# Kernel optimization log

Measured on AMD Instinct MI355X. Metric: run time of the kernel, lower is better.

Reference implementation:

```python
import math
import jax, jax.numpy as jnp
import numpy as np

D_MODEL = 128
NUM_HEADS = 8
FACTOR = 5


def setup_inputs() -> dict:
    key = jax.random.key(0)
    ks = jax.random.split(key, 9)
    B, L, dm = 2, 4096, D_MODEL
    s = 1.0 / math.sqrt(dm)
    return {
        "x": jax.random.normal(ks[0], (B, L, dm), dtype=jnp.float32),
        "Wq": jax.random.normal(ks[1], (dm, dm), dtype=jnp.float32) * s,
        "bq": jnp.zeros((dm,), jnp.float32),
        "Wk": jax.random.normal(ks[2], (dm, dm), dtype=jnp.float32) * s,
        "bk": jnp.zeros((dm,), jnp.float32),
        "Wv": jax.random.normal(ks[3], (dm, dm), dtype=jnp.float32) * s,
        "bv": jnp.zeros((dm,), jnp.float32),
        "Wo": jax.random.normal(ks[4], (dm, dm), dtype=jnp.float32) * s,
        "bo": jnp.zeros((dm,), jnp.float32),
    }


def reference(x, Wq, bq, Wk, bk, Wv, bv, Wo, bo):
    B, L, dm = x.shape
    H = NUM_HEADS
    D = dm // H
    inv_sqrt_d = 1.0 / math.sqrt(D)

    def split_heads(t):  # [B,L,dm] -> [B,H,L,D]
        return t.reshape(B, L, H, D).transpose(0, 2, 1, 3)

    Q = split_heads(x @ Wq + bq)
    K = split_heads(x @ Wk + bk)
    V = split_heads(x @ Wv + bv)

    # sample_k = min(L_K, int(log(L_K) * factor)); L is static under jit
    sample_k = min(L, int(math.log(L) * FACTOR))

    # _prob_QK: full scores, per-query stable exp, mean over queries, top-k keys
    scores_full = jnp.einsum("bhqd,bhkd->bhqk", Q, K) * inv_sqrt_d  # [B,H,L,L]
    m = jnp.max(scores_full, axis=-1, keepdims=True)
    e = jnp.exp(scores_full - m)
    mean_attn = jnp.mean(e, axis=2)  # [B,H,L_K]
    _, idx = jax.lax.top_k(mean_attn, sample_k)  # [B,H,sample_k]

    # gather sampled keys/values along the key axis
    Ks = jnp.take_along_axis(K, idx[..., None], axis=2)  # [B,H,s,D]
    Vs = jnp.take_along_axis(V, idx[..., None], axis=2)

    attn = jax.nn.softmax(jnp.einsum("bhqd,bhsd->bhqs", Q, Ks) * inv_sqrt_d, axis=-1)
    out = jnp.einsum("bhqs,bhsd->bhqd", attn, Vs)  # [B,H,L,D]
    out = out.transpose(0, 2, 1, 3).reshape(B, L, dm)
    return out @ Wo + bo
```

## Files before the change

### kernel.cpp

```cpp
#include <hip/hip_runtime.h>
#include <hip/hip_bf16.h>

#define L 4096
#define DM 128
#define NH 8
#define HD 16
#define NBH 16
#define SK 41
#define NSPLIT 8
#define SLICE (L/NSPLIT)
#define KK (SLICE/16)
#define QSCALE 0.36067376022224085f

typedef __attribute__((ext_vector_type(8))) short s16x8;
typedef __attribute__((ext_vector_type(4))) float f32x4;

#define MFMA16(A,B,C) __builtin_amdgcn_mfma_f32_16x16x32_bf16(A,B,C,0,0,0)

__device__ __forceinline__ float bf2f(unsigned short h){ return __uint_as_float(((unsigned)h)<<16); }
__device__ __forceinline__ unsigned short f2bf(float f){
  unsigned u = __float_as_uint(f);
  u += 0x7FFFu + ((u>>16)&1u);
  return (unsigned short)(u>>16);
}
__device__ __forceinline__ float fast_exp2(float x){
  float r;
  asm("v_exp_f32 %0, %1" : "=v"(r) : "v"(x));
  return r;
}

__global__ __launch_bounds__(256) void prep(
    const float* __restrict__ x,
    const float* __restrict__ Wq, const float* __restrict__ Wk,
    const float* __restrict__ Wv, const float* __restrict__ Wo,
    unsigned short* __restrict__ Xh, unsigned short* __restrict__ Xl,
    unsigned short* __restrict__ Wph, unsigned short* __restrict__ Wpl)
{
  const int t = threadIdx.x;
  const int blk = blockIdx.x;
  if (blk < 1024){
    const long base = (long)blk*1024 + t*4;
    float4 v = *(const float4*)(x + base);
    unsigned short h[4], lo[4];
    h[0]=f2bf(v.x); lo[0]=f2bf(v.x - bf2f(h[0]));
    h[1]=f2bf(v.y); lo[1]=f2bf(v.y - bf2f(h[1]));
    h[2]=f2bf(v.z); lo[2]=f2bf(v.z - bf2f(h[2]));
    h[3]=f2bf(v.w); lo[3]=f2bf(v.w - bf2f(h[3]));
    *(uint2*)(Xh+base) = *(uint2*)h;
    *(uint2*)(Xl+base) = *(uint2*)lo;
  } else {
    const int e = (blk-1024)*256 + t;
    const int p = e >> 14;
    const int idx = e & 16383;
    const int j = idx & 7;
    const int f = idx >> 3;
    const int n = f & 127;
    const int kcg = f >> 7;
    const int k = (kcg>>1)*16 + (kcg&1)*8 + j;
    const float* W = (p==0)?Wq:((p==1)?Wk:((p==2)?Wv:Wo));
    const float v = W[k*128 + n];
    const unsigned short h = f2bf(v);
    Wph[e] = h;
    Wpl[e] = f2bf(v - bf2f(h));
  }
}

__global__ __launch_bounds__(256) void proj_mfma(
    const unsigned short* __restrict__ Xh, const unsigned short* __restrict__ Xl,
    const unsigned short* __restrict__ Wph, const unsigned short* __restrict__ Wpl,
    const float* __restrict__ bq, const float* __restrict__ bk, const float* __restrict__ bv,
    unsigned short* __restrict__ Qh, unsigned short* __restrict__ Ql,
    unsigned short* __restrict__ Kh, unsigned short* __restrict__ Kl,
    float* __restrict__ Vo)
{
  const int p = blockIdx.y;
  const float* __restrict__ bias = (p==0)?bq:((p==1)?bk:bv);
  __shared__ __align__(16) unsigned short wh[16384];
  __shared__ __align__(16) unsigned short wl[16384];
  const int t = threadIdx.x;
  {
    const uint4* gh = (const uint4*)(Wph + (long)p*16384);
    const uint4* gl = (const uint4*)(Wpl + (long)p*16384);
    uint4* sh = (uint4*)wh; uint4* sl = (uint4*)wl;
#pragma unroll
    for (int i=0;i<8;++i){ sh[t + i*256] = gh[t + i*256]; sl[t + i*256] = gl[t + i*256]; }
  }
  __syncthreads();
  const int w = t>>6, l = t&63;
  const int lc = l&15, g = l>>4;
  const int mbase = blockIdx.x*64 + w*16;
  f32x4 acc[8];
#pragma unroll
  for (int nt=0;nt<8;++nt){ acc[nt][0]=0.f; acc[nt][1]=0.f; acc[nt][2]=0.f; acc[nt][3]=0.f; }
  const unsigned short* __restrict__ Asrc = (g<2)? Xh : Xl;
  const int koff = (g&1)*8;
  for (int kc=0; kc<8; ++kc){
    s16x8 a = *(const s16x8*)(Asrc + ((long)(mbase + lc))*128 + kc*16 + koff);
#pragma unroll
    for (int nt=0;nt<8;++nt){
      const int fi = (kc*2+(g&1))*128 + nt*16 + lc;
      s16x8 b1 = ((const s16x8*)wh)[fi];
      s16x8 b2 = ((const s16x8*)wl)[fi];
      acc[nt] = MFMA16(a, b1, acc[nt]);
      acc[nt] = MFMA16(a, b2, acc[nt]);
    }
  }
#pragma unroll
  for (int nt=0;nt<8;++nt){
    const float bb = bias[nt*16 + lc];
#pragma unroll
    for (int r=0;r<4;++r){
      const int row = mbase + g*4 + r;
      float v = acc[nt][r] + bb;
      const int b = row>>12, li = row&4095;
      const long o = (((long)(b*NH + nt))*L + li)*HD + lc;
      if (p==2){
        Vo[o] = v;
      } else {
        if (p==0) v *= QSCALE;
        const unsigned short h = f2bf(v);
        const unsigned short lo2 = f2bf(v - bf2f(h));
        if (p==0){ Qh[o]=h; Ql[o]=lo2; } else { Kh[o]=h; Kl[o]=lo2; }
      }
    }
  }
}

__global__ __launch_bounds__(256) void rowmax_k(
    const unsigned short* __restrict__ Qh, const unsigned short* __restrict__ Ql,
    const unsigned short* __restrict__ Kh, const unsigned short* __restrict__ Kl,
    float* __restrict__ mpart)
{
  const int bh = blockIdx.y, qt = blockIdx.x, ks = blockIdx.z;
  const int t = threadIdx.x, w = t>>6, l = t&63;
  const int half = (l>>4)&1, part = l>>5, lc = l&15;
  __shared__ __align__(16) unsigned short khs[SLICE*HD];
  __shared__ __align__(16) unsigned short kls[SLICE*HD];
  {
    const uint4* gh = (const uint4*)(Kh + ((long)bh*L + ks*SLICE)*HD);
    const uint4* gl = (const uint4*)(Kl + ((long)bh*L + ks*SLICE)*HD);
    uint4* sh = (uint4*)khs; uint4* sl = (uint4*)kls;
#pragma unroll
    for (int i=0;i<4;++i){ sh[t + i*256] = gh[t + i*256]; sl[t + i*256] = gl[t + i*256]; }
  }
  s16x8 aq[4];
  {
    const unsigned short* Qsrc = part ? Ql : Qh;
#pragma unroll
    for (int m=0;m<4;++m){
      const int row = qt*256 + w*64 + m*16 + lc;
      aq[m] = *(const s16x8*)(Qsrc + (((long)bh*L + row)*HD) + half*8);
    }
  }
  __syncthreads();
  f32x4 fz; fz[0]=0.f; fz[1]=0.f; fz[2]=0.f; fz[3]=0.f;
  f32x4 rmax[4];
#pragma unroll
  for (int m=0;m<4;++m){ rmax[m][0]=rmax[m][1]=rmax[m][2]=rmax[m][3]=-3.4e38f; }
  const int boff = lc*HD + half*8;
  f32x4 accA[4], accB[4];
  {
    s16x8 b1 = *(const s16x8*)(khs + boff);
    s16x8 b2 = *(const s16x8*)(kls + boff);
#pragma unroll
    for (int m=0;m<4;++m){ accA[m] = MFMA16(aq[m], b2, fz); accA[m] = MFMA16(aq[m], b1, accA[m]); }
  }
  for (int kk=0; kk<KK-2; kk+=2){
    {
      s16x8 b1 = *(const s16x8*)(khs + (kk+1)*256 + boff);
      s16x8 b2 = *(const s16x8*)(kls + (kk+1)*256 + boff);
#pragma unroll
      for (int m=0;m<4;++m){ accB[m] = MFMA16(aq[m], b2, fz); accB[m] = MFMA16(aq[m], b1, accB[m]); }
    }
#pragma unroll
    for (int m=0;m<4;++m)
#pragma unroll
      for (int r=0;r<4;++r) rmax[m][r] = fmaxf(rmax[m][r], accA[m][r]);
    {
      s16x8 b1 = *(const s16x8*)(khs + (kk+2)*256 + boff);
      s16x8 b2 = *(const s16x8*)(kls + (kk+2)*256 + boff);
#pragma unroll
      for (int m=0;m<4;++m){ accA[m] = MFMA16(aq[m], b2, fz); accA[m] = MFMA16(aq[m], b1, accA[m]); }
    }
#pragma unroll
    for (int m=0;m<4;++m)
#pragma unroll
      for (int r=0;r<4;++r) rmax[m][r] = fmaxf(rmax[m][r], accB[m][r]);
  }
  {
    s16x8 b1 = *(const s16x8*)(khs + (KK-1)*256 + boff);
    s16x8 b2 = *(const s16x8*)(kls + (KK-1)*256 + boff);
#pragma unroll
    for (int m=0;m<4;++m){ accB[m] = MFMA16(aq[m], b2, fz); accB[m] = MFMA16(aq[m], b1, accB[m]); }
  }
#pragma unroll
  for (int m=0;m<4;++m)
#pragma unroll
    for (int r=0;r<4;++r) rmax[m][r] = fmaxf(fmaxf(rmax[m][r], accA[m][r]), accB[m][r]);
#pragma unroll
  for (int m=0;m<4;++m){
#pragma unroll
    for (int r=0;r<4;++r){
      float v = rmax[m][r];
      v = fmaxf(v, __shfl_xor(v, 1));
      v = fmaxf(v, __shfl_xor(v, 2));
      v = fmaxf(v, __shfl_xor(v, 4));
      v = fmaxf(v, __shfl_xor(v, 8));
      rmax[m][r] = v;
    }
  }
  if (lc == 0){
    const int q4 = l>>4;
#pragma unroll
    for (int m=0;m<4;++m){
#pragma unroll
      for (int r=0;r<4;++r){
        const int row = qt*256 + w*64 + m*16 + q4*4 + r;
        mpart[((long)ks*NBH + bh)*L + row] = rmax[m][r];
      }
    }
  }
}

__global__ __launch_bounds__(256) void colexp_k(
    const unsigned short* __restrict__ Kh, const unsigned short* __restrict__ Kl,
    const unsigned short* __restrict__ Qh, const unsigned short* __restrict__ Ql,
    const float* __restrict__ mpart, float* __restrict__ cspart)
{
  const int bh = blockIdx.y, kt = blockIdx.x, qs = blockIdx.z;
  const int t = threadIdx.x, w = t>>6, l = t&63;
  const int half = (l>>4)&1, part = l>>5, lc = l&15;
  __shared__ __align__(16) unsigned short qhs[SLICE*HD];
  __shared__ __align__(16) unsigned short qls[SLICE*HD];
  __shared__ float ws_s[SLICE];
  {
    const uint4* gh = (const uint4*)(Qh + ((long)bh*L + qs*SLICE)*HD);
    const uint4* gl = (const uint4*)(Ql + ((long)bh*L + qs*SLICE)*HD);
    uint4* sh = (uint4*)qhs; uint4* sl = (uint4*)qls;
#pragma unroll
    for (int i=0;i<4;++i){ sh[t + i*256] = gh[t + i*256]; sl[t + i*256] = gl[t + i*256]; }
#pragma unroll
    for (int rr=0; rr<2; ++rr){
      const int tq = t + rr*256;
      const long qi = (long)bh*L + qs*SLICE + tq;
      float m = -3.4e38f;
#pragma unroll
      for (int p=0;p<NSPLIT;++p) m = fmaxf(m, mpart[(long)p*NBH*L + qi]);
      ws_s[tq] = fast_exp2(-m);
    }
  }
  s16x8 ak[4];
  {
    const unsigned short* Ksrc = part ? Kl : Kh;
#pragma unroll
    for (int m=0;m<4;++m){
      const int key = kt*256 + w*64 + m*16 + lc;
      ak[m] = *(const s16x8*)(Ksrc + (((long)bh*L + key)*HD) + half*8);
    }
  }
  __syncthreads();
  f32x4 fz; fz[0]=0.f; fz[1]=0.f; fz[2]=0.f; fz[3]=0.f;
  f32x4 csum[4];
#pragma unroll
  for (int m=0;m<4;++m){ csum[m][0]=0.f; csum[m][1]=0.f; csum[m][2]=0.f; csum[m][3]=0.f; }
  const int boff = lc*HD + half*8;
  f32x4 accA[4], accB[4];
  {
    s16x8 b1 = *(const s16x8*)(qhs + boff);
    s16x8 b2 = *(const s16x8*)(qls + boff);
#pragma unroll
    for (int m=0;m<4;++m){ accA[m] = MFMA16(ak[m], b2, fz); accA[m] = MFMA16(ak[m], b1, accA[m]); }
  }
  for (int kk=0; kk<KK-2; kk+=2){
    {
      s16x8 b1 = *(const s16x8*)(qhs + (kk+1)*256 + boff);
      s16x8 b2 = *(const s16x8*)(qls + (kk+1)*256 + boff);
#pragma unroll
      for (int m=0;m<4;++m){ accB[m] = MFMA16(ak[m], b2, fz); accB[m] = MFMA16(ak[m], b1, accB[m]); }
    }
    {
      const float cw = ws_s[kk*16 + lc];
#pragma unroll
      for (int m=0;m<4;++m)
#pragma unroll
        for (int r=0;r<4;++r)
          csum[m][r] = fmaf(fast_exp2(accA[m][r]), cw, csum[m][r]);
    }
    {
      s16x8 b1 = *(const s16x8*)(qhs + (kk+2)*256 + boff);
      s16x8 b2 = *(const s16x8*)(qls + (kk+2)*256 + boff);
#pragma unroll
      for (int m=0;m<4;++m){ accA[m] = MFMA16(ak[m], b2, fz); accA[m] = MFMA16(ak[m], b1, accA[m]); }
    }
    {
      const float cw = ws_s[(kk+1)*16 + lc];
#pragma unroll
      for (int m=0;m<4;++m)
#pragma unroll
        for (int r=0;r<4;++r)
          csum[m][r] = fmaf(fast_exp2(accB[m][r]), cw, csum[m][r]);
    }
  }
  {
    s16x8 b1 = *(const s16x8*)(qhs + (KK-1)*256 + boff);
    s16x8 b2 = *(const s16x8*)(qls + (KK-1)*256 + boff);
#pragma unroll
    for (int m=0;m<4;++m){ accB[m] = MFMA16(ak[m], b2, fz); accB[m] = MFMA16(ak[m], b1, accB[m]); }
  }
  {
    const float cwA = ws_s[(KK-2)*16 + lc];
    const float cwB = ws_s[(KK-1)*16 + lc];
#pragma unroll
    for (int m=0;m<4;++m)
#pragma unroll
      for (int r=0;r<4;++r){
        csum[m][r] = fmaf(fast_exp2(accA[m][r]), cwA, csum[m][r]);
        csum[m][r] = fmaf(fast_exp2(accB[m][r]), cwB, csum[m][r]);
      }
  }
#pragma unroll
  for (int m=0;m<4;++m){
#pragma unroll
    for (int r=0;r<4;++r){
      float v = csum[m][r];
      v += __shfl_xor(v, 1);
      v += __shfl_xor(v, 2);
      v += __shfl_xor(v, 4);
      v += __shfl_xor(v, 8);
      csum[m][r] = v;
    }
  }
  if (lc == 0){
    const int k4 = l>>4;
#pragma unroll
    for (int m=0;m<4;++m){
#pragma unroll
      for (int r=0;r<4;++r){
        const int key = kt*256 + w*64 + m*16 + k4*4 + r;
        cspart[((long)qs*NBH + bh)*L + key] = csum[m][r];
      }
    }
  }
}

__global__ __launch_bounds__(256) void topk_gather(
    const float* __restrict__ cspart,
    const unsigned short* __restrict__ Kh, const unsigned short* __restrict__ Kl,
    const float* __restrict__ V,
    float* __restrict__ Ks, float* __restrict__ Vs)
{
  const int bh = blockIdx.x;
  const int t = threadIdx.x;
  __shared__ float vals[4096];
  __shared__ unsigned hist[2048];
  __shared__ unsigned suf[256];
  __shared__ int meta[4];
  __shared__ int sel[SK];
  __shared__ int sorted[SK];
  __shared__ int tiei[4096];

  for (int i=t; i<1024; i+=256){
    float4 s = {0.f,0.f,0.f,0.f};
#pragma unroll
    for (int p=0;p<NSPLIT;++p){
      float4 v = *(const float4*)(cspart + ((long)p*NBH + bh)*L + i*4);
      s.x += v.x; s.y += v.y; s.z += v.z; s.w += v.w;
    }
    *(float4*)&vals[i*4] = s;
  }
  __syncthreads();

  int target = SK;
  unsigned B1 = 0, P2 = 0, T = 0;
#pragma unroll
  for (int pass=0; pass<3; ++pass){
    const int nb = (pass<2) ? 2048 : 1024;
    const int chunk = nb >> 8;
    for (int i=t;i<nb;i+=256) hist[i]=0u;
    __syncthreads();
    for (int i=t;i<4096;i+=256){
      const unsigned u = __float_as_uint(vals[i]);
      bool ok; int bk;
      if (pass==0){ ok = true;              bk = (int)(u>>21); }
      else if (pass==1){ ok = ((u>>21)==B1); bk = (int)((u>>10)&0x7FFu); }
      else { ok = ((u>>10)==P2);            bk = (int)(u&0x3FFu); }
      if (ok) atomicAdd(&hist[bk], 1u);
    }
    __syncthreads();
    {
      unsigned c=0;
#pragma unroll
      for (int b=0;b<8;++b) if (b<chunk) c += hist[t*chunk+b];
      suf[t]=c;
    }
    __syncthreads();
    for (int off=1; off<256; off<<=1){
      unsigned add = (t+off<256)? suf[t+off] : 0u;
      __syncthreads();
      suf[t] += add;
      __syncthreads();
    }
    {
      const unsigned mysuf = suf[t];
      const unsigned nxt = (t==255)?0u:suf[t+1];
      if (mysuf >= (unsigned)target && nxt < (unsigned)target){
        unsigned running = nxt;
        for (int b=t*chunk+chunk-1; b>=t*chunk; --b){
          const unsigned h = hist[b];
          if (running + h >= (unsigned)target){ meta[0]=b; meta[1]=(int)running; break; }
          running += h;
        }
      }
    }
    __syncthreads();
    const unsigned B = (unsigned)meta[0];
    target -= meta[1];
    if (pass==0) B1 = B;
    else if (pass==1) P2 = (B1<<11)|B;
    else T = (P2<<10)|B;
    __syncthreads();
  }
  if (t==0){ meta[2]=0; meta[3]=0; }
  __syncthreads();
  for (int i=t;i<4096;i+=256){
    const unsigned u = __float_as_uint(vals[i]);
    if (u > T){ int p = atomicAdd(&meta[2],1); sel[p]=i; }
    else if (u == T){ int p = atomicAdd(&meta[3],1); tiei[p]=i; }
  }
  __syncthreads();
  const int ngt = meta[2];
  const int ntie = meta[3];
  for (int j=t; j<ntie; j+=256){
    const int x = tiei[j];
    int rk=0;
    for (int k=0;k<ntie;++k) rk += (tiei[k] < x);
    if (rk < target) sel[ngt+rk] = x;
  }
  __syncthreads();
  if (t<SK){
    int x=sel[t]; int rk=0;
    for (int j=0;j<SK;++j) rk += (sel[j]<x);
    sorted[rk]=x;
  }
  __syncthreads();
  for (int i=t;i<SK*HD;i+=256){
    const int j=i>>4, dd=i&15;
    const int key=sorted[j];
    const long src=((long)bh*L+key)*HD+dd;
    Ks[(long)bh*SK*HD+i]=bf2f(Kh[src])+bf2f(Kl[src]);
    Vs[(long)bh*SK*HD+i]=V[src];
  }
}

__global__ __launch_bounds__(256) void sattn(
    const unsigned short* __restrict__ Qh, const unsigned short* __restrict__ Ql,
    const float* __restrict__ Ks, const float* __restrict__ Vs,
    unsigned short* __restrict__ AOh, unsigned short* __restrict__ AOl)
{
  const int bh = blockIdx.y, qb = blockIdx.x;
  const int t = threadIdx.x;
  __shared__ float ks[SK*HD], vs[SK*HD];
  for (int i=t; i<SK*HD; i+=256){
    ks[i] = Ks[(long)bh*SK*HD + i];
    vs[i] = Vs[(long)bh*SK*HD + i];
  }
  __syncthreads();
  const int q = qb*128 + (t>>1);
  const int half = t&1;
  const long qo = ((long)bh*L + q)*HD;
  float qv[16];
  {
    s16x8 h0 = *(const s16x8*)(Qh+qo);
    s16x8 h1 = *(const s16x8*)(Qh+qo+8);
    s16x8 l0 = *(const s16x8*)(Ql+qo);
    s16x8 l1 = *(const s16x8*)(Ql+qo+8);
#pragma unroll
    for (int d=0; d<8; ++d){
      qv[d]   = bf2f((unsigned short)h0[d]) + bf2f((unsigned short)l0[d]);
      qv[d+8] = bf2f((unsigned short)h1[d]) + bf2f((unsigned short)l1[d]);
    }
  }
  float sc[21];
#pragma unroll
  for (int i=0;i<21;++i){
    const int j = half + 2*i;
    if (j < SK){
      float4 k0 = *(const float4*)&ks[j*HD+0];
      float4 k1 = *(const float4*)&ks[j*HD+4];
      float4 k2 = *(const float4*)&ks[j*HD+8];
      float4 k3 = *(const float4*)&ks[j*HD+12];
      float s = qv[0]*k0.x;
      s = fmaf(qv[1],k0.y,s); s = fmaf(qv[2],k0.z,s); s = fmaf(qv[3],k0.w,s);
      s = fmaf(qv[4],k1.x,s); s = fmaf(qv[5],k1.y,s); s = fmaf(qv[6],k1.z,s); s = fmaf(qv[7],k1.w,s);
      s = fmaf(qv[8],k2.x,s); s = fmaf(qv[9],k2.y,s); s = fmaf(qv[10],k2.z,s); s = fmaf(qv[11],k2.w,s);
      s = fmaf(qv[12],k3.x,s); s = fmaf(qv[13],k3.y,s); s = fmaf(qv[14],k3.z,s); s = fmaf(qv[15],k3.w,s);
      sc[i] = s;
    } else {
      sc[i] = -3.4e38f;
    }
  }
  float m = sc[0];
#pragma unroll
  for (int i=1;i<21;++i) m = fmaxf(m, sc[i]);
  float lrun = 0.f, out[16];
#pragma unroll
  for (int d=0; d<16; ++d) out[d] = 0.f;
#pragma unroll
  for (int i=0;i<21;++i){
    const int j = half + 2*i;
    const float p = fast_exp2(sc[i] - m);
    lrun += p;
    if (j < SK){
      float4 v0 = *(const float4*)&vs[j*HD+0];
      float4 v1 = *(const float4*)&vs[j*HD+4];
      float4 v2 = *(const float4*)&vs[j*HD+8];
      float4 v3 = *(const float4*)&vs[j*HD+12];
      out[0]=fmaf(p,v0.x,out[0]); out[1]=fmaf(p,v0.y,out[1]); out[2]=fmaf(p,v0.z,out[2]); out[3]=fmaf(p,v0.w,out[3]);
      out[4]=fmaf(p,v1.x,out[4]); out[5]=fmaf(p,v1.y,out[5]); out[6]=fmaf(p,v1.z,out[6]); out[7]=fmaf(p,v1.w,out[7]);
      out[8]=fmaf(p,v2.x,out[8]); out[9]=fmaf(p,v2.y,out[9]); out[10]=fmaf(p,v2.z,out[10]); out[11]=fmaf(p,v2.w,out[11]);
      out[12]=fmaf(p,v3.x,out[12]); out[13]=fmaf(p,v3.y,out[13]); out[14]=fmaf(p,v3.z,out[14]); out[15]=fmaf(p,v3.w,out[15]);
    }
  }
  const float mo = __shfl_xor(m, 1);
  const float lo = __shfl_xor(lrun, 1);
  const float mm = fmaxf(m, mo);
  const float cs_ = fast_exp2(m - mm);
  const float co_ = fast_exp2(mo - mm);
  const float ltot = fmaf(lrun, cs_, lo*co_);
  const float inv = 1.f / ltot;
#pragma unroll
  for (int d=0; d<16; ++d){
    const float ov = __shfl_xor(out[d], 1);
    out[d] = fmaf(out[d]*cs_, inv, ov*co_*inv);
  }
  if (half == 0){
    const int b = bh>>3, h = bh&7;
    const long row = (long)b*L + q;
    unsigned short hv[16], lv[16];
#pragma unroll
    for (int d=0; d<16; ++d){
      const float v = out[d];
      hv[d] = f2bf(v);
      lv[d] = f2bf(v - bf2f(hv[d]));
    }
    unsigned short* oh = AOh + row*DM + h*HD;
    unsigned short* ol = AOl + row*DM + h*HD;
    *(uint4*)(oh)   = *(uint4*)(hv);
    *(uint4*)(oh+8) = *(uint4*)(hv+8);
    *(uint4*)(ol)   = *(uint4*)(lv);
    *(uint4*)(ol+8) = *(uint4*)(lv+8);
  }
}

__global__ __launch_bounds__(256) void outproj_mfma(
    const unsigned short* __restrict__ AOh, const unsigned short* __restrict__ AOl,
    const unsigned short* __restrict__ Wph, const unsigned short* __restrict__ Wpl,
    const float* __restrict__ bo, float* __restrict__ out)
{
  __shared__ __align__(16) unsigned short wh[16384];
  __shared__ __align__(16) unsigned short wl[16384];
  const int t = threadIdx.x;
  {
    const uint4* gh = (const uint4*)(Wph + (long)3*16384);
    const uint4* gl = (const uint4*)(Wpl + (long)3*16384);
    uint4* sh = (uint4*)wh; uint4* sl = (uint4*)wl;
#pragma unroll
    for (int i=0;i<8;++i){ sh[t + i*256] = gh[t + i*256]; sl[t + i*256] = gl[t + i*256]; }
  }
  __syncthreads();
  const int w = t>>6, l = t&63;
  const int lc = l&15, g = l>>4;
  const int mbase = blockIdx.x*64 + w*16;
  f32x4 acc[8];
#pragma unroll
  for (int nt=0;nt<8;++nt){ acc[nt][0]=0.f; acc[nt][1]=0.f; acc[nt][2]=0.f; acc[nt][3]=0.f; }
  const unsigned short* __restrict__ Asrc = (g<2)? AOh : AOl;
  const int koff = (g&1)*8;
  for (int kc=0; kc<8; ++kc){
    s16x8 a = *(const s16x8*)(Asrc + ((long)(mbase + lc))*128 + kc*16 + koff);
#pragma unroll
    for (int nt=0;nt<8;++nt){
      const int fi = (kc*2+(g&1))*128 + nt*16 + lc;
      s16x8 b1 = ((const s16x8*)wh)[fi];
      s16x8 b2 = ((const s16x8*)wl)[fi];
      acc[nt] = MFMA16(a, b1, acc[nt]);
      acc[nt] = MFMA16(a, b2, acc[nt]);
    }
  }
#pragma unroll
  for (int nt=0;nt<8;++nt){
    const float bb = bo[nt*16 + lc];
#pragma unroll
    for (int r=0;r<4;++r){
      const int row = mbase + g*4 + r;
      out[(long)row*DM + nt*16 + lc] = acc[nt][r] + bb;
    }
  }
}

extern "C" void kernel_launch(void* const* d_in, const int* in_sizes, int n_in,
                              void* d_out, int out_size, void* d_ws, size_t ws_size,
                              hipStream_t stream)
{
  const float* x  = (const float*)d_in[0];
  const float* Wq = (const float*)d_in[1];
  const float* bq = (const float*)d_in[2];
  const float* Wk = (const float*)d_in[3];
  const float* bk = (const float*)d_in[4];
  const float* Wv = (const float*)d_in[5];
  const float* bv = (const float*)d_in[6];
  const float* Wo = (const float*)d_in[7];
  const float* bo = (const float*)d_in[8];
  float* out = (float*)d_out;

  char* wsp = (char*)d_ws;
  size_t o = 0;
  auto alloc = [&](size_t bytes)->char*{
    char* p = wsp + o; o += (bytes + 255) & ~(size_t)255; return p;
  };
  unsigned short* Qh = (unsigned short*)alloc((size_t)NBH*L*HD*2);
  unsigned short* Ql = (unsigned short*)alloc((size_t)NBH*L*HD*2);
  unsigned short* Kh = (unsigned short*)alloc((size_t)NBH*L*HD*2);
  unsigned short* Kl = (unsigned short*)alloc((size_t)NBH*L*HD*2);
  float* Vv    = (float*)alloc((size_t)NBH*L*HD*4);
  float* mpart = (float*)alloc((size_t)NSPLIT*NBH*L*4);
  float* cspart= (float*)alloc((size_t)NSPLIT*NBH*L*4);
  float* Ks    = (float*)alloc((size_t)NBH*SK*HD*4);
  float* Vs    = (float*)alloc((size_t)NBH*SK*HD*4);
  unsigned short* Xh  = (unsigned short*)alloc((size_t)2*L*DM*2);
  unsigned short* Xl  = (unsigned short*)alloc((size_t)2*L*DM*2);
  unsigned short* AOh = (unsigned short*)alloc((size_t)2*L*DM*2);
  unsigned short* AOl = (unsigned short*)alloc((size_t)2*L*DM*2);
  unsigned short* Wph = (unsigned short*)alloc((size_t)4*16384*2);
  unsigned short* Wpl = (unsigned short*)alloc((size_t)4*16384*2);

  prep<<<1280,256,0,stream>>>(x,Wq,Wk,Wv,Wo,Xh,Xl,Wph,Wpl);
  proj_mfma<<<dim3(128,3),256,0,stream>>>(Xh,Xl,Wph,Wpl,bq,bk,bv,Qh,Ql,Kh,Kl,Vv);
  rowmax_k<<<dim3(16,16,NSPLIT),256,0,stream>>>(Qh,Ql,Kh,Kl,mpart);
  colexp_k<<<dim3(16,16,NSPLIT),256,0,stream>>>(Kh,Kl,Qh,Ql,mpart,cspart);
  topk_gather<<<16,256,0,stream>>>(cspart,Kh,Kl,Vv,Ks,Vs);
  sattn<<<dim3(32,16),256,0,stream>>>(Qh,Ql,Ks,Vs,AOh,AOl);
  outproj_mfma<<<128,256,0,stream>>>(AOh,AOl,Wph,Wpl,bo,out);
}
```

Baseline: 132.1 us.

## Use bit-trick exp2 for column sums, then re-rank top candidates exactly

Replaces the hardware exp in the full column-exp pass with a cheap integer bit-trick exp2 approximation. Top-k then selects 192 candidate keys from these approximate sums. A new kernel recomputes exact column sums for only those candidates, and a final kernel picks the true top 41. The aim is to cut transcendental cost in the dominant L×L pass while keeping selection exact. The cost is two extra kernel launches, and a true top-41 key could fall outside the approximate top 192.

```diff
diff --git a/kernel.cpp b/kernel.cpp
--- a/kernel.cpp
+++ b/kernel.cpp
@@ -7,6 +7,7 @@
 #define HD 16
 #define NBH 16
 #define SK 41
+#define NC 192
 #define NSPLIT 8
 #define SLICE (L/NSPLIT)
 #define KK (SLICE/16)
@@ -27,6 +28,11 @@
   float r;
   asm("v_exp_f32 %0, %1" : "=v"(r) : "v"(x));
   return r;
+}
+__device__ __forceinline__ float approx_exp2(float x){
+  x = fmaxf(x, -120.f);
+  const float y = fmaf(x, 8388608.f, 1064986823.f);
+  return __int_as_float((int)y);
 }
 
 __global__ __launch_bounds__(256) void prep(
@@ -284,7 +290,7 @@
       for (int m=0;m<4;++m)
 #pragma unroll
         for (int r=0;r<4;++r)
-          csum[m][r] = fmaf(fast_exp2(accA[m][r]), cw, csum[m][r]);
+          csum[m][r] = fmaf(approx_exp2(accA[m][r]), cw, csum[m][r]);
     }
     {
       s16x8 b1 = *(const s16x8*)(qhs + (kk+2)*256 + boff);
@@ -298,7 +304,7 @@
       for (int m=0;m<4;++m)
 #pragma unroll
         for (int r=0;r<4;++r)
-          csum[m][r] = fmaf(fast_exp2(accB[m][r]), cw, csum[m][r]);
+          csum[m][r] = fmaf(approx_exp2(accB[m][r]), cw, csum[m][r]);
     }
   }
   {
@@ -314,8 +320,8 @@
     for (int m=0;m<4;++m)
 #pragma unroll
       for (int r=0;r<4;++r){
-        csum[m][r] = fmaf(fast_exp2(accA[m][r]), cwA, csum[m][r]);
-        csum[m][r] = fmaf(fast_exp2(accB[m][r]), cwB, csum[m][r]);
+        csum[m][r] = fmaf(approx_exp2(accA[m][r]), cwA, csum[m][r]);
+        csum[m][r] = fmaf(approx_exp2(accB[m][r]), cwB, csum[m][r]);
       }
   }
 #pragma unroll
@@ -343,11 +349,11 @@
   }
 }
 
-__global__ __launch_bounds__(256) void topk_gather(
+__global__ __launch_bounds__(256) void topk_cand(
     const float* __restrict__ cspart,
     const unsigned short* __restrict__ Kh, const unsigned short* __restrict__ Kl,
-    const float* __restrict__ V,
-    float* __restrict__ Ks, float* __restrict__ Vs)
+    int* __restrict__ candIdx,
+    unsigned short* __restrict__ Kch, unsigned short* __restrict__ Kcl)
 {
   const int bh = blockIdx.x;
   const int t = threadIdx.x;
@@ -355,8 +361,7 @@
   __shared__ unsigned hist[2048];
   __shared__ unsigned suf[256];
   __shared__ int meta[4];
-  __shared__ int sel[SK];
-  __shared__ int sorted[SK];
+  __shared__ int sel[NC];
   __shared__ int tiei[4096];
 
   for (int i=t; i<1024; i+=256){
@@ -370,7 +375,7 @@
   }
   __syncthreads();
 
-  int target = SK;
+  int target = NC;
   unsigned B1 = 0, P2 = 0, T = 0;
 #pragma unroll
   for (int pass=0; pass<3; ++pass){
@@ -437,10 +442,130 @@
     if (rk < target) sel[ngt+rk] = x;
   }
   __syncthreads();
-  if (t<SK){
-    int x=sel[t]; int rk=0;
-    for (int j=0;j<SK;++j) rk += (sel[j]<x);
-    sorted[rk]=x;
+  if (t < NC) candIdx[bh*NC + t] = sel[t];
+  for (int i=t; i<NC*HD; i+=256){
+    const int j=i>>4, dd=i&15;
+    const int key=sel[j];
+    const long src=((long)bh*L+key)*HD+dd;
+    const long dst=((long)bh*NC+j)*HD+dd;
+    Kch[dst]=Kh[src];
+    Kcl[dst]=Kl[src];
+  }
+}
+
+__global__ __launch_bounds__(256) void colexp_exact(
+    const unsigned short* __restrict__ Kch, const unsigned short* __restrict__ Kcl,
+    const unsigned short* __restrict__ Qh, const unsigned short* __restrict__ Ql,
+    const float* __restrict__ mpart, float* __restrict__ cse)
+{
+  const int qs = blockIdx.x, bh = blockIdx.y;
+  const int t = threadIdx.x, w = t>>6, l = t&63;
+  const int half = (l>>4)&1, part = l>>5, lc = l&15;
+  __shared__ __align__(16) unsigned short qhs[SLICE*HD];
+  __shared__ __align__(16) unsigned short qls[SLICE*HD];
+  __shared__ float ws_s[SLICE];
+  {
+    const uint4* gh = (const uint4*)(Qh + ((long)bh*L + qs*SLICE)*HD);
+    const uint4* gl = (const uint4*)(Ql + ((long)bh*L + qs*SLICE)*HD);
+    uint4* sh = (uint4*)qhs; uint4* sl = (uint4*)qls;
+#pragma unroll
+    for (int i=0;i<4;++i){ sh[t + i*256] = gh[t + i*256]; sl[t + i*256] = gl[t + i*256]; }
+#pragma unroll
+    for (int rr=0; rr<2; ++rr){
+      const int tq = t + rr*256;
+      const long qi = (long)bh*L + qs*SLICE + tq;
+      float m = -3.4e38f;
+#pragma unroll
+      for (int p=0;p<NSPLIT;++p) m = fmaxf(m, mpart[(long)p*NBH*L + qi]);
+      ws_s[tq] = fast_exp2(-m);
+    }
+  }
+  s16x8 ak[3];
+  {
+    const unsigned short* Ksrc = part ? Kcl : Kch;
+#pragma unroll
+    for (int m=0;m<3;++m){
+      const int row = w*48 + m*16 + lc;
+      ak[m] = *(const s16x8*)(Ksrc + ((long)bh*NC + row)*HD + half*8);
+    }
+  }
+  __syncthreads();
+  f32x4 fz; fz[0]=0.f; fz[1]=0.f; fz[2]=0.f; fz[3]=0.f;
+  f32x4 csum[3];
+#pragma unroll
+  for (int m=0;m<3;++m){ csum[m][0]=0.f; csum[m][1]=0.f; csum[m][2]=0.f; csum[m][3]=0.f; }
+  const int boff = lc*HD + half*8;
+  for (int kk=0; kk<KK; ++kk){
+    s16x8 b1 = *(const s16x8*)(qhs + kk*256 + boff);
+    s16x8 b2 = *(const s16x8*)(qls + kk*256 + boff);
+    const float cw = ws_s[kk*16 + lc];
+#pragma unroll
+    for (int m=0;m<3;++m){
+      f32x4 acc = MFMA16(ak[m], b2, fz);
+      acc = MFMA16(ak[m], b1, acc);
+#pragma unroll
+      for (int r=0;r<4;++r)
+        csum[m][r] = fmaf(fast_exp2(acc[r]), cw, csum[m][r]);
+    }
+  }
+#pragma unroll
+  for (int m=0;m<3;++m){
+#pragma unroll
+    for (int r=0;r<4;++r){
+      float v = csum[m][r];
+      v += __shfl_xor(v, 1);
+      v += __shfl_xor(v, 2);
+      v += __shfl_xor(v, 4);
+      v += __shfl_xor(v, 8);
+      csum[m][r] = v;
+    }
+  }
+  if (lc == 0){
+    const int k4 = l>>4;
+#pragma unroll
+    for (int m=0;m<3;++m){
+#pragma unroll
+      for (int r=0;r<4;++r){
+        const int c = w*48 + m*16 + k4*4 + r;
+        cse[((long)qs*NBH + bh)*NC + c] = csum[m][r];
+      }
+    }
+  }
+}
+
+__global__ __launch_bounds__(256) void topk_final(
+    const float* __restrict__ cse, const int* __restrict__ candIdx,
+    const unsigned short* __restrict__ Kh, const unsigned short* __restrict__ Kl,
+    const float* __restrict__ V,
+    float* __restrict__ Ks, float* __restrict__ Vs)
+{
+  const int bh = blockIdx.x;
+  const int t = threadIdx.x;
+  __shared__ float v[NC];
+  __shared__ int idx[NC];
+  __shared__ unsigned char fl[NC];
+  __shared__ int sorted[SK];
+  if (t < NC){
+    float s = 0.f;
+#pragma unroll
+    for (int p=0;p<NSPLIT;++p) s += cse[((long)p*NBH + bh)*NC + t];
+    v[t] = s;
+    idx[t] = candIdx[bh*NC + t];
+  }
+  __syncthreads();
+  if (t < NC){
+    const float mv = v[t]; const int mi = idx[t];
+    int rank = 0;
+    for (int j=0;j<NC;++j)
+      rank += (v[j] > mv) || (v[j] == mv && idx[j] < mi);
+    fl[t] = (rank < SK) ? 1 : 0;
+  }
+  __syncthreads();
+  if (t < NC && fl[t]){
+    const int mi = idx[t];
+    int pos = 0;
+    for (int j=0;j<NC;++j) pos += (fl[j] && idx[j] < mi);
+    sorted[pos] = mi;
   }
   __syncthreads();
   for (int i=t;i<SK*HD;i+=256){
@@ -625,6 +750,10 @@
   float* Vv    = (float*)alloc((size_t)NBH*L*HD*4);
   float* mpart = (float*)alloc((size_t)NSPLIT*NBH*L*4);
   float* cspart= (float*)alloc((size_t)NSPLIT*NBH*L*4);
+  int*   candI = (int*)alloc((size_t)NBH*NC*4);
+  unsigned short* Kch = (unsigned short*)alloc((size_t)NBH*NC*HD*2);
+  unsigned short* Kcl = (unsigned short*)alloc((size_t)NBH*NC*HD*2);
+  float* cse   = (float*)alloc((size_t)NSPLIT*NBH*NC*4);
   float* Ks    = (float*)alloc((size_t)NBH*SK*HD*4);
   float* Vs    = (float*)alloc((size_t)NBH*SK*HD*4);
   unsigned short* Xh  = (unsigned short*)alloc((size_t)2*L*DM*2);
@@ -638,7 +767,9 @@
   proj_mfma<<<dim3(128,3),256,0,stream>>>(Xh,Xl,Wph,Wpl,bq,bk,bv,Qh,Ql,Kh,Kl,Vv);
   rowmax_k<<<dim3(16,16,NSPLIT),256,0,stream>>>(Qh,Ql,Kh,Kl,mpart);
   colexp_k<<<dim3(16,16,NSPLIT),256,0,stream>>>(Kh,Kl,Qh,Ql,mpart,cspart);
-  topk_gather<<<16,256,0,stream>>>(cspart,Kh,Kl,Vv,Ks,Vs);
+  topk_cand<<<16,256,0,stream>>>(cspart,Kh,Kl,candI,Kch,Kcl);
+  colexp_exact<<<dim3(8,16),256,0,stream>>>(Kch,Kcl,Qh,Ql,mpart,cse);
+  topk_final<<<16,256,0,stream>>>(cse,candI,Kh,Kl,Vv,Ks,Vs);
   sattn<<<dim3(32,16),256,0,stream>>>(Qh,Ql,Ks,Vs,AOh,AOl);
   outproj_mfma<<<128,256,0,stream>>>(AOh,AOl,Wph,Wpl,bo,out);
 }
```

After: 162.6 us. 23.0% more time.
